# Kernel optimization log

Measured on AMD Instinct MI355X. Metric: run time of the kernel, lower is better.

## Reference

```python
import jax, jax.numpy as jnp
import numpy as np

N_NODES = 50000
N_EDGES = 500000
N_GRAPHS = 256
D_IN, D_H1, D_H2, D_H3, D_OUT = 768, 256, 128, 64, 2


def _glorot(key, shape):
    fan_in, fan_out = shape[1], shape[0]
    lim = float(np.sqrt(6.0 / (fan_in + fan_out)))
    return jax.random.uniform(key, shape, jnp.float32, -lim, lim)


def setup_inputs() -> dict:
    key = jax.random.key(0)
    ks = jax.random.split(key, 12)
    x = jax.random.normal(ks[0], (N_NODES, D_IN), jnp.float32)
    edge_index = jax.random.randint(ks[1], (2, N_EDGES), 0, N_NODES, jnp.int64)
    batch = jnp.sort(jax.random.randint(ks[2], (N_NODES,), 0, N_GRAPHS, jnp.int64))
    return {
        "x": x,
        "edge_index": edge_index,
        "batch": batch,
        # SAGEConv1: out = lin_l(mean_aggr) + lin_r(x); bias only on lin_l (PyG default)
        "W1_l": _glorot(ks[3], (D_H1, D_IN)),
        "b1_l": jnp.zeros((D_H1,), jnp.float32),
        "W1_r": _glorot(ks[4], (D_H1, D_IN)),
        # SAGEConv2
        "W2_l": _glorot(ks[5], (D_H2, D_H1)),
        "b2_l": jnp.zeros((D_H2,), jnp.float32),
        "W2_r": _glorot(ks[6], (D_H2, D_H1)),
        # MLP head
        "W3": _glorot(ks[7], (D_H3, D_H2)),
        "b3": jnp.zeros((D_H3,), jnp.float32),
        "W4": _glorot(ks[8], (D_OUT, D_H3)),
        "b4": jnp.zeros((D_OUT,), jnp.float32),
    }


def _sage_conv(x, src, dst, deg_inv, W_l, b_l, W_r):
    # mean aggregation of neighbor features: scatter-add then divide by in-degree
    aggr = jax.ops.segment_sum(x[src], dst, num_segments=N_NODES)  # [N, d]
    aggr = aggr * deg_inv[:, None]
    return aggr @ W_l.T + b_l + x @ W_r.T


def reference(x, edge_index, batch, W1_l, b1_l, W1_r, W2_l, b2_l, W2_r, W3, b3, W4, b4):
    src, dst = edge_index[0], edge_index[1]
    deg = jax.ops.segment_sum(jnp.ones((N_EDGES,), x.dtype), dst, num_segments=N_NODES)
    deg_inv = jnp.where(deg > 0, 1.0 / jnp.maximum(deg, 1.0), 0.0)

    h = jax.nn.relu(_sage_conv(x, src, dst, deg_inv, W1_l, b1_l, W1_r))
    h = jax.nn.relu(_sage_conv(h, src, dst, deg_inv, W2_l, b2_l, W2_r))

    # global_mean_pool over graph ids
    pooled = jax.ops.segment_sum(h, batch, num_segments=N_GRAPHS)  # [G, 128]
    cnt = jax.ops.segment_sum(jnp.ones((N_NODES,), h.dtype), batch, num_segments=N_GRAPHS)
    pooled = pooled / jnp.maximum(cnt, 1.0)[:, None]

    # dropout is identity in eval mode
    h = pooled @ W3.T + b3
    h = h @ W4.T + b4
    return jax.nn.softmax(h, axis=-1)
```

## Files before the change

### kernel.cpp

```cpp
#include <hip/hip_runtime.h>
#include <cstdint>
#include <cstddef>

#define N_NODES 50000
#define N_EDGES 500000
#define N_GRAPHS 256
#define D_IN 768
#define D_H1 256
#define D_H2 128

typedef __attribute__((ext_vector_type(8))) __bf16 bf16x8;
typedef __attribute__((ext_vector_type(4))) float f32x4;

__device__ __forceinline__ float bf2f(uint32_t u) {
    union { uint32_t i; float f; } v; v.i = u << 16; return v.f;
}
__device__ __forceinline__ uint32_t f2bf(float f) {
    union { float f; uint32_t i; } v; v.f = f;
    uint32_t u = v.i;
    return (u + 0x7FFFu + ((u >> 16) & 1u)) >> 16;
}

__device__ __forceinline__ void pack_chunk(const float* __restrict__ p,
                                           uint16_t* __restrict__ out, int c) {
    float4 u = *(const float4*)p, v = *(const float4*)(p + 4);
    uint4 o;
    o.x = f2bf(u.x) | (f2bf(u.y) << 16);
    o.y = f2bf(u.z) | (f2bf(u.w) << 16);
    o.z = f2bf(v.x) | (f2bf(v.y) << 16);
    o.w = f2bf(v.z) | (f2bf(v.w) << 16);
    *(uint4*)(out + (size_t)c * 8) = o;
}

#define PACKA_BLKS 18750
#define PACKW1_BLKS 192
#define PACKW2_BLKS 32
#define HIST_BLKS 1954
__global__ __launch_bounds__(256) void k_pack_hist(
    const float* __restrict__ x, uint16_t* __restrict__ xp,
    const float* __restrict__ W1l, const float* __restrict__ W1r, uint16_t* __restrict__ W1p,
    const float* __restrict__ W2l, const float* __restrict__ W2r, uint16_t* __restrict__ W2p,
    const int* __restrict__ e_dst, int* __restrict__ deg)
{
    int b = blockIdx.x;
    if (b < PACKA_BLKS) {
        int c = b * 256 + threadIdx.x;
        int l = c & 63, t = c >> 6;
        int kt = t % 24, mt = t / 24;
        int fr = l & 15, fq = l >> 4;
        pack_chunk(x + (size_t)(mt * 16 + fr) * 768 + kt * 32 + fq * 8, xp, c);
    } else if (b < PACKA_BLKS + PACKW1_BLKS) {
        int c = (b - PACKA_BLKS) * 256 + threadIdx.x;
        int l = c & 63, t = c >> 6;
        int kt = t % 24, mt = t / 24;
        int fr = l & 15, fq = l >> 4;
        int row = mt * 16 + fr;
        const float* src = (row < 256) ? (W1l + (size_t)row * 768)
                                       : (W1r + (size_t)(row - 256) * 768);
        pack_chunk(src + kt * 32 + fq * 8, W1p, c);
    } else if (b < PACKA_BLKS + PACKW1_BLKS + PACKW2_BLKS) {
        int c = (b - PACKA_BLKS - PACKW1_BLKS) * 256 + threadIdx.x;
        int l = c & 63, t = c >> 6;
        int kt = t % 8, mt = t / 8;
        int fr = l & 15, fq = l >> 4;
        int row = mt * 16 + fr;
        const float* src = (row < 128) ? (W2l + (size_t)row * 256)
                                       : (W2r + (size_t)(row - 128) * 256);
        pack_chunk(src + kt * 32 + fq * 8, W2p, c);
    } else {
        int e = (b - PACKA_BLKS - PACKW1_BLKS - PACKW2_BLKS) * 256 + threadIdx.x;
        if (e < N_EDGES) atomicAdd(&deg[e_dst[e]], 1);
    }
}

__global__ void k_scan1(const int* __restrict__ deg, int* __restrict__ row_ex,
                        int* __restrict__ bsum, int n) {
    __shared__ int buf[256];
    int t = threadIdx.x, i = blockIdx.x * 256 + t;
    int v = (i < n) ? deg[i] : 0;
    buf[t] = v; __syncthreads();
    for (int off = 1; off < 256; off <<= 1) {
        int u = (t >= off) ? buf[t - off] : 0;
        __syncthreads(); buf[t] += u; __syncthreads();
    }
    if (i < n) row_ex[i] = buf[t] - v;
    if (t == 255) bsum[blockIdx.x] = buf[255];
}
__global__ void k_scan23(const int* __restrict__ deg, const int* __restrict__ bsum,
                         int* __restrict__ row_start, float* __restrict__ deg_inv,
                         int n, int nb) {
    __shared__ int buf[256];
    int t = threadIdx.x;
    int v = (t < nb) ? bsum[t] : 0;
    buf[t] = v; __syncthreads();
    for (int off = 1; off < 256; off <<= 1) {
        int u = (t >= off) ? buf[t - off] : 0;
        __syncthreads(); buf[t] += u; __syncthreads();
    }
    int b = blockIdx.x;
    int boff = buf[b] - ((b < nb) ? bsum[b] : 0);
    int i = b * 256 + t;
    if (i < n) {
        row_start[i] += boff;
        int d = deg[i];
        deg_inv[i] = (d > 0) ? (1.0f / (float)d) : 0.0f;
    }
    if (b == 0 && t == 0) row_start[n] = N_EDGES;
}

#define G1_BLKS 784
__global__ __launch_bounds__(256, 2) void k_gemm1_fill(
    const uint16_t* __restrict__ Ap, const uint16_t* __restrict__ Bp,
    uint16_t* __restrict__ Cl, uint16_t* __restrict__ Cr,
    const int* __restrict__ e_src, const int* __restrict__ e_dst,
    const int* __restrict__ row_start, int* __restrict__ cursor,
    int* __restrict__ csr_src)
{
    if (blockIdx.x >= G1_BLKS) {
        int e = (blockIdx.x - G1_BLKS) * 256 + threadIdx.x;
        if (e < N_EDGES) {
            int d = e_dst[e];
            int pos = row_start[d] + atomicAdd(&cursor[d], 1);
            csr_src[pos] = e_src[e];
        }
        return;
    }
    const int i = blockIdx.x;
    const int pr = (i >> 4) * 8 + (i & 7);
    const int half = (i >> 3) & 1;
    if (pr >= 391) return;
    const int KT = 24, M = N_NODES;
    const int tid = threadIdx.x;
    const int wave = tid >> 6, lane = tid & 63;
    const int fr = lane & 15, fq = lane >> 4;
    const int bm = pr * 128;
    const int wm = (wave >> 1) * 64, wn = (wave & 1) * 128;
    const int mtiles = (M + 15) >> 4;

    const bf16x8* ap[4];
    const bf16x8* bp[8];
    #pragma unroll
    for (int mi = 0; mi < 4; ++mi) {
        int mt = ((bm + wm) >> 4) + mi;
        if (mt > mtiles - 1) mt = mtiles - 1;
        ap[mi] = (const bf16x8*)Ap + (size_t)mt * KT * 64 + lane;
    }
    #pragma unroll
    for (int ni = 0; ni < 8; ++ni) {
        int nt = ((half * 256 + wn) >> 4) + ni;
        bp[ni] = (const bf16x8*)Bp + (size_t)nt * KT * 64 + lane;
    }

    f32x4 acc[4][8] = {};
    bf16x8 a0[4], b0[8], a1[4], b1[8];

    auto lA = [&](int kt, bf16x8* d) {
        #pragma unroll
        for (int mi = 0; mi < 4; ++mi) d[mi] = ap[mi][kt * 64];
    };
    auto lB = [&](int kt, bf16x8* d) {
        #pragma unroll
        for (int ni = 0; ni < 8; ++ni) d[ni] = bp[ni][kt * 64];
    };
    auto step = [&](bf16x8* a, bf16x8* b) {
        #pragma unroll
        for (int mi = 0; mi < 4; ++mi)
            #pragma unroll
            for (int ni = 0; ni < 8; ++ni)
                acc[mi][ni] = __builtin_amdgcn_mfma_f32_16x16x32_bf16(
                    a[mi], b[ni], acc[mi][ni], 0, 0, 0);
    };

    lA(0, a0); lB(0, b0);
    for (int ks = 0; ks < KT; ks += 2) {
        lA(ks + 1, a1); lB(ks + 1, b1);
        step(a0, b0);
        if (ks + 2 < KT) { lA(ks + 2, a0); lB(ks + 2, b0); }
        step(a1, b1);
    }

    uint16_t* __restrict__ C = half ? Cr : Cl;
    #pragma unroll
    for (int mi = 0; mi < 4; ++mi) {
        #pragma unroll
        for (int r = 0; r < 4; ++r) {
            int row = bm + wm + mi * 16 + fq * 4 + r;
            if (row >= M) continue;
            #pragma unroll
            for (int ni = 0; ni < 8; ++ni) {
                int col = wn + ni * 16 + fr;
                C[(size_t)row * 256 + col] = (uint16_t)f2bf(acc[mi][ni][r]);
            }
        }
    }
}

__global__ __launch_bounds__(256, 2) void k_mgemm(
    const uint16_t* __restrict__ Ap, const uint16_t* __restrict__ Bp,
    uint16_t* __restrict__ C, int M, int N, int KT)
{
    const int tid = threadIdx.x;
    const int wave = tid >> 6, lane = tid & 63;
    const int fr = lane & 15, fq = lane >> 4;
    const int bn = blockIdx.x * 256, bm = blockIdx.y * 128;
    const int wm = (wave >> 1) * 64, wn = (wave & 1) * 128;
    const int mtiles = (M + 15) >> 4;

    const bf16x8* ap[4];
    const bf16x8* bp[8];
    #pragma unroll
    for (int mi = 0; mi < 4; ++mi) {
        int mt = ((bm + wm) >> 4) + mi;
        if (mt > mtiles - 1) mt = mtiles - 1;
        ap[mi] = (const bf16x8*)Ap + (size_t)mt * KT * 64 + lane;
    }
    #pragma unroll
    for (int ni = 0; ni < 8; ++ni) {
        int nt = ((bn + wn) >> 4) + ni;
        bp[ni] = (const bf16x8*)Bp + (size_t)nt * KT * 64 + lane;
    }

    f32x4 acc[4][8] = {};
    bf16x8 a0[4], b0[8], a1[4], b1[8];

    auto lA = [&](int kt, bf16x8* d) {
        #pragma unroll
        for (int mi = 0; mi < 4; ++mi) d[mi] = ap[mi][kt * 64];
    };
    auto lB = [&](int kt, bf16x8* d) {
        #pragma unroll
        for (int ni = 0; ni < 8; ++ni) d[ni] = bp[ni][kt * 64];
    };
    auto step = [&](bf16x8* a, bf16x8* b) {
        #pragma unroll
        for (int mi = 0; mi < 4; ++mi)
            #pragma unroll
            for (int ni = 0; ni < 8; ++ni)
                acc[mi][ni] = __builtin_amdgcn_mfma_f32_16x16x32_bf16(
                    a[mi], b[ni], acc[mi][ni], 0, 0, 0);
    };

    lA(0, a0); lB(0, b0);
    for (int ks = 0; ks < KT; ks += 2) {
        lA(ks + 1, a1); lB(ks + 1, b1);
        step(a0, b0);
        if (ks + 2 < KT) { lA(ks + 2, a0); lB(ks + 2, b0); }
        step(a1, b1);
    }

    #pragma unroll
    for (int mi = 0; mi < 4; ++mi) {
        #pragma unroll
        for (int r = 0; r < 4; ++r) {
            int row = bm + wm + mi * 16 + fq * 4 + r;
            if (row >= M) continue;
            #pragma unroll
            for (int ni = 0; ni < 8; ++ni) {
                int col = bn + wn + ni * 16 + fr;
                C[(size_t)row * N + col] = (uint16_t)f2bf(acc[mi][ni][r]);
            }
        }
    }
}

__global__ __launch_bounds__(256) void k_agg1(
    const uint16_t* __restrict__ yl, const uint16_t* __restrict__ yr,
    const int* __restrict__ row_start, const int* __restrict__ csr,
    const float* __restrict__ deg_inv, const float* __restrict__ bias,
    uint16_t* __restrict__ h1p)
{
    int node = blockIdx.x * 8 + (threadIdx.x >> 5);
    if (node >= N_NODES) return;
    int c = threadIdx.x & 31;
    int s = row_start[node], e = row_start[node + 1];
    float a[8] = {};
    int p = s;
    for (; p + 1 < e; p += 2) {
        uint4 t0 = *(const uint4*)(yl + (size_t)csr[p] * 256 + c * 8);
        uint4 t1 = *(const uint4*)(yl + (size_t)csr[p + 1] * 256 + c * 8);
        a[0] += bf2f(t0.x & 0xFFFF) + bf2f(t1.x & 0xFFFF);
        a[1] += bf2f(t0.x >> 16)    + bf2f(t1.x >> 16);
        a[2] += bf2f(t0.y & 0xFFFF) + bf2f(t1.y & 0xFFFF);
        a[3] += bf2f(t0.y >> 16)    + bf2f(t1.y >> 16);
        a[4] += bf2f(t0.z & 0xFFFF) + bf2f(t1.z & 0xFFFF);
        a[5] += bf2f(t0.z >> 16)    + bf2f(t1.z >> 16);
        a[6] += bf2f(t0.w & 0xFFFF) + bf2f(t1.w & 0xFFFF);
        a[7] += bf2f(t0.w >> 16)    + bf2f(t1.w >> 16);
    }
    if (p < e) {
        uint4 t0 = *(const uint4*)(yl + (size_t)csr[p] * 256 + c * 8);
        a[0] += bf2f(t0.x & 0xFFFF); a[1] += bf2f(t0.x >> 16);
        a[2] += bf2f(t0.y & 0xFFFF); a[3] += bf2f(t0.y >> 16);
        a[4] += bf2f(t0.z & 0xFFFF); a[5] += bf2f(t0.z >> 16);
        a[6] += bf2f(t0.w & 0xFFFF); a[7] += bf2f(t0.w >> 16);
    }
    float w = deg_inv[node];
    uint4 tx = *(const uint4*)(yr + (size_t)node * 256 + c * 8);
    float4 b0 = *(const float4*)(bias + c * 8);
    float4 b1 = *(const float4*)(bias + c * 8 + 4);
    float v0 = fmaxf(a[0] * w + bf2f(tx.x & 0xFFFF) + b0.x, 0.f);
    float v1 = fmaxf(a[1] * w + bf2f(tx.x >> 16)    + b0.y, 0.f);
    float v2 = fmaxf(a[2] * w + bf2f(tx.y & 0xFFFF) + b0.z, 0.f);
    float v3 = fmaxf(a[3] * w + bf2f(tx.y >> 16)    + b0.w, 0.f);
    float v4 = fmaxf(a[4] * w + bf2f(tx.z & 0xFFFF) + b1.x, 0.f);
    float v5 = fmaxf(a[5] * w + bf2f(tx.z >> 16)    + b1.y, 0.f);
    float v6 = fmaxf(a[6] * w + bf2f(tx.w & 0xFFFF) + b1.z, 0.f);
    float v7 = fmaxf(a[7] * w + bf2f(tx.w >> 16)    + b1.w, 0.f);
    uint4 o;
    o.x = f2bf(v0) | (f2bf(v1) << 16);
    o.y = f2bf(v2) | (f2bf(v3) << 16);
    o.z = f2bf(v4) | (f2bf(v5) << 16);
    o.w = f2bf(v6) | (f2bf(v7) << 16);
    uint32_t addr = (((node >> 4) * 8 + (c >> 2)) * 64 + (c & 3) * 16 + (node & 15));
    *(uint4*)(h1p + (size_t)addr * 8) = o;
}

__global__ __launch_bounds__(256) void k_agg2(
    const uint16_t* __restrict__ y, const int* __restrict__ row_start,
    const int* __restrict__ csr, const float* __restrict__ deg_inv,
    const float* __restrict__ bias, float* __restrict__ out)
{
    int node = blockIdx.x * 4 + (threadIdx.x >> 6);
    if (node >= N_NODES) return;
    int lane = threadIdx.x & 63;
    int s = row_start[node], e = row_start[node + 1];
    float a0 = 0.f, a1 = 0.f;
    int p = s;
    for (; p + 1 < e; p += 2) {
        uint32_t t0 = *(const uint32_t*)(y + (size_t)csr[p] * 256 + lane * 2);
        uint32_t t1 = *(const uint32_t*)(y + (size_t)csr[p + 1] * 256 + lane * 2);
        a0 += bf2f(t0 & 0xFFFF) + bf2f(t1 & 0xFFFF);
        a1 += bf2f(t0 >> 16)    + bf2f(t1 >> 16);
    }
    if (p < e) {
        uint32_t t0 = *(const uint32_t*)(y + (size_t)csr[p] * 256 + lane * 2);
        a0 += bf2f(t0 & 0xFFFF);
        a1 += bf2f(t0 >> 16);
    }
    float w = deg_inv[node];
    uint32_t tx = *(const uint32_t*)(y + (size_t)node * 256 + 128 + lane * 2);
    float2 b = *(const float2*)(bias + lane * 2);
    float2 o;
    o.x = fmaxf(a0 * w + bf2f(tx & 0xFFFF) + b.x, 0.f);
    o.y = fmaxf(a1 * w + bf2f(tx >> 16)    + b.y, 0.f);
    *(float2*)(out + (size_t)node * 128 + lane * 2) = o;
}

__global__ void k_poolhead(const float* __restrict__ h2, const int* __restrict__ batch,
                           const float* __restrict__ W3, const float* __restrict__ b3,
                           const float* __restrict__ W4, const float* __restrict__ b4,
                           float* __restrict__ out)
{
    int g = blockIdx.x;
    __shared__ int s_lo, s_hi;
    __shared__ float p[128];
    __shared__ float hid[64];
    __shared__ float logit[2];
    int t = threadIdx.x;
    if (t == 0) {
        int lo = 0, hi = N_NODES;
        while (lo < hi) { int m = (lo + hi) >> 1; if (batch[m] < g) lo = m + 1; else hi = m; }
        s_lo = lo;
        int lo2 = lo, hi2 = N_NODES;
        while (lo2 < hi2) { int m = (lo2 + hi2) >> 1; if (batch[m] < g + 1) lo2 = m + 1; else hi2 = m; }
        s_hi = lo2;
    }
    __syncthreads();
    float sum = 0.f;
    for (int i = s_lo; i < s_hi; ++i) sum += h2[(size_t)i * D_H2 + t];
    int cnt = s_hi - s_lo;
    p[t] = sum / (float)(cnt > 0 ? cnt : 1);
    __syncthreads();
    if (t < 64) {
        float s = b3[t];
        #pragma unroll 4
        for (int k = 0; k < 128; ++k) s = fmaf(p[k], W3[t * 128 + k], s);
        hid[t] = s;
    }
    __syncthreads();
    if (t < 2) {
        float l = b4[t];
        for (int k = 0; k < 64; ++k) l = fmaf(hid[k], W4[t * 64 + k], l);
        logit[t] = l;
    }
    __syncthreads();
    if (t == 0) {
        float m = fmaxf(logit[0], logit[1]);
        float e0 = expf(logit[0] - m), e1 = expf(logit[1] - m);
        float inv = 1.0f / (e0 + e1);
        out[g * 2 + 0] = e0 * inv;
        out[g * 2 + 1] = e1 * inv;
    }
}

extern "C" void kernel_launch(void* const* d_in, const int* in_sizes, int n_in,
                              void* d_out, int out_size, void* d_ws, size_t ws_size,
                              hipStream_t stream)
{
    const float* x     = (const float*)d_in[0];
    const int*   ei    = (const int*)d_in[1];
    const int*   batch = (const int*)d_in[2];
    const float* W1l   = (const float*)d_in[3];
    const float* b1l   = (const float*)d_in[4];
    const float* W1r   = (const float*)d_in[5];
    const float* W2l   = (const float*)d_in[6];
    const float* b2l   = (const float*)d_in[7];
    const float* W2r   = (const float*)d_in[8];
    const float* W3    = (const float*)d_in[9];
    const float* b3    = (const float*)d_in[10];
    const float* W4    = (const float*)d_in[11];
    const float* b4    = (const float*)d_in[12];
    float* out = (float*)d_out;

    const int* e_src = ei;
    const int* e_dst = ei + N_EDGES;

    char* ws = (char*)d_ws;
    size_t off = 0;
    auto alloc = [&](size_t bytes) -> void* {
        void* p = ws + off;
        off = (off + bytes + 255) & ~(size_t)255;
        return p;
    };
    int*      deg       = (int*)alloc((size_t)2 * N_NODES * 4);
    int*      cursor    = deg + N_NODES;
    int*      row_start = (int*)alloc((size_t)(N_NODES + 1) * 4);
    int*      csr_src   = (int*)alloc((size_t)N_EDGES * 4);
    float*    deg_inv   = (float*)alloc((size_t)N_NODES * 4);
    int*      bsum      = (int*)alloc(256 * 4);
    uint16_t* W1p       = (uint16_t*)alloc((size_t)512 * 768 * 2);
    uint16_t* W2p       = (uint16_t*)alloc((size_t)256 * 256 * 2);
    uint16_t* xp        = (uint16_t*)alloc((size_t)N_NODES * D_IN * 2);
    uint16_t* y1        = (uint16_t*)alloc((size_t)N_NODES * 512 * 2);
    uint16_t* h1p       = (uint16_t*)alloc((size_t)N_NODES * 256 * 2);

    uint16_t* y1l = y1;
    uint16_t* y1r = y1 + (size_t)N_NODES * 256;
    uint16_t* y2 = xp;
    float*    h2 = (float*)(xp + (size_t)N_NODES * 256);

    hipMemsetAsync(deg, 0, (size_t)2 * N_NODES * 4, stream);

    k_pack_hist<<<PACKA_BLKS + PACKW1_BLKS + PACKW2_BLKS + HIST_BLKS, 256, 0, stream>>>(
        x, xp, W1l, W1r, W1p, W2l, W2r, W2p, e_dst, deg);

    int nscan = (N_NODES + 255) / 256;
    k_scan1<<<nscan, 256, 0, stream>>>(deg, row_start, bsum, N_NODES);
    k_scan23<<<nscan, 256, 0, stream>>>(deg, bsum, row_start, deg_inv, N_NODES, nscan);

    k_gemm1_fill<<<G1_BLKS + HIST_BLKS, 256, 0, stream>>>(
        xp, W1p, y1l, y1r, e_src, e_dst, row_start, cursor, csr_src);
    k_agg1<<<(N_NODES + 7) / 8, 256, 0, stream>>>(y1l, y1r, row_start, csr_src, deg_inv, b1l, h1p);

    dim3 g2(1, (N_NODES + 127) / 128);
    k_mgemm<<<g2, 256, 0, stream>>>(h1p, W2p, y2, N_NODES, 256, 8);
    k_agg2<<<(N_NODES + 3) / 4, 256, 0, stream>>>(y2, row_start, csr_src, deg_inv, b2l, h2);

    k_poolhead<<<N_GRAPHS, 128, 0, stream>>>(h2, batch, W3, b3, W4, b4, out);
}
```

Measured before the change: 486.8 us.

## Fuse two-pass scan into one kernel with cross-block spin wait; unroll gathers by four

The two scan kernels become a single kernel. Each block publishes its block sum to a global array, and every block spin-waits on those sums to compute its own offset, which removes one launch. The scan also seeds the cursor array with the row start, so the CSR fill does one atomic instead of an extra row_start load. The aggregation loops are unrolled from two to four neighbours to put more loads in flight. The spin wait assumes all 196 scan blocks are co-resident, which holds on this GPU but is not guaranteed in general.

```diff
diff --git a/kernel.cpp b/kernel.cpp
--- a/kernel.cpp
+++ b/kernel.cpp
@@ -35,7 +35,7 @@
 #define PACKA_BLKS 18750
 #define PACKW1_BLKS 192
 #define PACKW2_BLKS 32
-#define HIST_BLKS 1954
+#define HIST256 1954
 __global__ __launch_bounds__(256) void k_pack_hist(
     const float* __restrict__ x, uint16_t* __restrict__ xp,
     const float* __restrict__ W1l, const float* __restrict__ W1r, uint16_t* __restrict__ W1p,
@@ -73,54 +73,53 @@
     }
 }
 
-__global__ void k_scan1(const int* __restrict__ deg, int* __restrict__ row_ex,
-                        int* __restrict__ bsum, int n) {
+__global__ __launch_bounds__(256) void k_scan(
+    const int* __restrict__ deg, int* __restrict__ row_start, int* __restrict__ cursor,
+    float* __restrict__ deg_inv, int* __restrict__ bsum, int n, int nb)
+{
     __shared__ int buf[256];
-    int t = threadIdx.x, i = blockIdx.x * 256 + t;
+    __shared__ int bbuf[256];
+    int t = threadIdx.x, b = blockIdx.x, i = b * 256 + t;
     int v = (i < n) ? deg[i] : 0;
     buf[t] = v; __syncthreads();
     for (int off = 1; off < 256; off <<= 1) {
         int u = (t >= off) ? buf[t - off] : 0;
         __syncthreads(); buf[t] += u; __syncthreads();
     }
-    if (i < n) row_ex[i] = buf[t] - v;
-    if (t == 255) bsum[blockIdx.x] = buf[255];
-}
-__global__ void k_scan23(const int* __restrict__ deg, const int* __restrict__ bsum,
-                         int* __restrict__ row_start, float* __restrict__ deg_inv,
-                         int n, int nb) {
-    __shared__ int buf[256];
-    int t = threadIdx.x;
-    int v = (t < nb) ? bsum[t] : 0;
-    buf[t] = v; __syncthreads();
+    if (t == 255) atomicExch(&bsum[b], buf[255] + 1);
+    int w = 0;
+    if (t < nb) {
+        do { w = atomicAdd(&bsum[t], 0); } while (w == 0);
+        w -= 1;
+    }
+    bbuf[t] = w; __syncthreads();
     for (int off = 1; off < 256; off <<= 1) {
-        int u = (t >= off) ? buf[t - off] : 0;
-        __syncthreads(); buf[t] += u; __syncthreads();
-    }
-    int b = blockIdx.x;
-    int boff = buf[b] - ((b < nb) ? bsum[b] : 0);
-    int i = b * 256 + t;
+        int u = (t >= off) ? bbuf[t - off] : 0;
+        __syncthreads(); bbuf[t] += u; __syncthreads();
+    }
+    int base = (b > 0) ? bbuf[b - 1] : 0;
     if (i < n) {
-        row_start[i] += boff;
-        int d = deg[i];
-        deg_inv[i] = (d > 0) ? (1.0f / (float)d) : 0.0f;
+        int rs = base + buf[t] - v;
+        row_start[i] = rs;
+        cursor[i] = rs;
+        deg_inv[i] = (v > 0) ? (1.0f / (float)v) : 0.0f;
     }
     if (b == 0 && t == 0) row_start[n] = N_EDGES;
 }
 
 #define G1_BLKS 784
+#define FILL_BLKS 1954
 __global__ __launch_bounds__(256, 2) void k_gemm1_fill(
     const uint16_t* __restrict__ Ap, const uint16_t* __restrict__ Bp,
     uint16_t* __restrict__ Cl, uint16_t* __restrict__ Cr,
     const int* __restrict__ e_src, const int* __restrict__ e_dst,
-    const int* __restrict__ row_start, int* __restrict__ cursor,
-    int* __restrict__ csr_src)
+    int* __restrict__ cursor, int* __restrict__ csr_src)
 {
     if (blockIdx.x >= G1_BLKS) {
         int e = (blockIdx.x - G1_BLKS) * 256 + threadIdx.x;
         if (e < N_EDGES) {
             int d = e_dst[e];
-            int pos = row_start[d] + atomicAdd(&cursor[d], 1);
+            int pos = atomicAdd(&cursor[d], 1);
             csr_src[pos] = e_src[e];
         }
         return;
@@ -129,13 +128,13 @@
     const int pr = (i >> 4) * 8 + (i & 7);
     const int half = (i >> 3) & 1;
     if (pr >= 391) return;
-    const int KT = 24, M = N_NODES;
+    const int KT = 24;
     const int tid = threadIdx.x;
     const int wave = tid >> 6, lane = tid & 63;
     const int fr = lane & 15, fq = lane >> 4;
     const int bm = pr * 128;
     const int wm = (wave >> 1) * 64, wn = (wave & 1) * 128;
-    const int mtiles = (M + 15) >> 4;
+    const int mtiles = (N_NODES + 15) >> 4;
 
     const bf16x8* ap[4];
     const bf16x8* bp[8];
@@ -185,7 +184,7 @@
         #pragma unroll
         for (int r = 0; r < 4; ++r) {
             int row = bm + wm + mi * 16 + fq * 4 + r;
-            if (row >= M) continue;
+            if (row >= N_NODES) continue;
             #pragma unroll
             for (int ni = 0; ni < 8; ++ni) {
                 int col = wn + ni * 16 + fr;
@@ -275,25 +274,21 @@
     int s = row_start[node], e = row_start[node + 1];
     float a[8] = {};
     int p = s;
-    for (; p + 1 < e; p += 2) {
-        uint4 t0 = *(const uint4*)(yl + (size_t)csr[p] * 256 + c * 8);
-        uint4 t1 = *(const uint4*)(yl + (size_t)csr[p + 1] * 256 + c * 8);
-        a[0] += bf2f(t0.x & 0xFFFF) + bf2f(t1.x & 0xFFFF);
-        a[1] += bf2f(t0.x >> 16)    + bf2f(t1.x >> 16);
-        a[2] += bf2f(t0.y & 0xFFFF) + bf2f(t1.y & 0xFFFF);
-        a[3] += bf2f(t0.y >> 16)    + bf2f(t1.y >> 16);
-        a[4] += bf2f(t0.z & 0xFFFF) + bf2f(t1.z & 0xFFFF);
-        a[5] += bf2f(t0.z >> 16)    + bf2f(t1.z >> 16);
-        a[6] += bf2f(t0.w & 0xFFFF) + bf2f(t1.w & 0xFFFF);
-        a[7] += bf2f(t0.w >> 16)    + bf2f(t1.w >> 16);
-    }
-    if (p < e) {
-        uint4 t0 = *(const uint4*)(yl + (size_t)csr[p] * 256 + c * 8);
+    auto accum = [&](uint4 t0) {
         a[0] += bf2f(t0.x & 0xFFFF); a[1] += bf2f(t0.x >> 16);
         a[2] += bf2f(t0.y & 0xFFFF); a[3] += bf2f(t0.y >> 16);
         a[4] += bf2f(t0.z & 0xFFFF); a[5] += bf2f(t0.z >> 16);
         a[6] += bf2f(t0.w & 0xFFFF); a[7] += bf2f(t0.w >> 16);
-    }
+    };
+    for (; p + 3 < e; p += 4) {
+        uint4 t0 = *(const uint4*)(yl + (size_t)csr[p]     * 256 + c * 8);
+        uint4 t1 = *(const uint4*)(yl + (size_t)csr[p + 1] * 256 + c * 8);
+        uint4 t2 = *(const uint4*)(yl + (size_t)csr[p + 2] * 256 + c * 8);
+        uint4 t3 = *(const uint4*)(yl + (size_t)csr[p + 3] * 256 + c * 8);
+        accum(t0); accum(t1); accum(t2); accum(t3);
+    }
+    for (; p < e; ++p)
+        accum(*(const uint4*)(yl + (size_t)csr[p] * 256 + c * 8));
     float w = deg_inv[node];
     uint4 tx = *(const uint4*)(yr + (size_t)node * 256 + c * 8);
     float4 b0 = *(const float4*)(bias + c * 8);
@@ -326,13 +321,15 @@
     int s = row_start[node], e = row_start[node + 1];
     float a0 = 0.f, a1 = 0.f;
     int p = s;
-    for (; p + 1 < e; p += 2) {
-        uint32_t t0 = *(const uint32_t*)(y + (size_t)csr[p] * 256 + lane * 2);
+    for (; p + 3 < e; p += 4) {
+        uint32_t t0 = *(const uint32_t*)(y + (size_t)csr[p]     * 256 + lane * 2);
         uint32_t t1 = *(const uint32_t*)(y + (size_t)csr[p + 1] * 256 + lane * 2);
-        a0 += bf2f(t0 & 0xFFFF) + bf2f(t1 & 0xFFFF);
-        a1 += bf2f(t0 >> 16)    + bf2f(t1 >> 16);
-    }
-    if (p < e) {
+        uint32_t t2 = *(const uint32_t*)(y + (size_t)csr[p + 2] * 256 + lane * 2);
+        uint32_t t3 = *(const uint32_t*)(y + (size_t)csr[p + 3] * 256 + lane * 2);
+        a0 += bf2f(t0 & 0xFFFF) + bf2f(t1 & 0xFFFF) + bf2f(t2 & 0xFFFF) + bf2f(t3 & 0xFFFF);
+        a1 += bf2f(t0 >> 16)    + bf2f(t1 >> 16)    + bf2f(t2 >> 16)    + bf2f(t3 >> 16);
+    }
+    for (; p < e; ++p) {
         uint32_t t0 = *(const uint32_t*)(y + (size_t)csr[p] * 256 + lane * 2);
         a0 += bf2f(t0 & 0xFFFF);
         a1 += bf2f(t0 >> 16);
@@ -422,12 +419,12 @@
         off = (off + bytes + 255) & ~(size_t)255;
         return p;
     };
-    int*      deg       = (int*)alloc((size_t)2 * N_NODES * 4);
-    int*      cursor    = deg + N_NODES;
+    int*      deg       = (int*)alloc((size_t)(N_NODES + 256) * 4);
+    int*      bsum      = deg + N_NODES;
     int*      row_start = (int*)alloc((size_t)(N_NODES + 1) * 4);
+    int*      cursor    = (int*)alloc((size_t)N_NODES * 4);
     int*      csr_src   = (int*)alloc((size_t)N_EDGES * 4);
     float*    deg_inv   = (float*)alloc((size_t)N_NODES * 4);
-    int*      bsum      = (int*)alloc(256 * 4);
     uint16_t* W1p       = (uint16_t*)alloc((size_t)512 * 768 * 2);
     uint16_t* W2p       = (uint16_t*)alloc((size_t)256 * 256 * 2);
     uint16_t* xp        = (uint16_t*)alloc((size_t)N_NODES * D_IN * 2);
@@ -439,17 +436,16 @@
     uint16_t* y2 = xp;
     float*    h2 = (float*)(xp + (size_t)N_NODES * 256);
 
-    hipMemsetAsync(deg, 0, (size_t)2 * N_NODES * 4, stream);
-
-    k_pack_hist<<<PACKA_BLKS + PACKW1_BLKS + PACKW2_BLKS + HIST_BLKS, 256, 0, stream>>>(
+    hipMemsetAsync(deg, 0, (size_t)(N_NODES + 256) * 4, stream);
+
+    k_pack_hist<<<PACKA_BLKS + PACKW1_BLKS + PACKW2_BLKS + HIST256, 256, 0, stream>>>(
         x, xp, W1l, W1r, W1p, W2l, W2r, W2p, e_dst, deg);
 
     int nscan = (N_NODES + 255) / 256;
-    k_scan1<<<nscan, 256, 0, stream>>>(deg, row_start, bsum, N_NODES);
-    k_scan23<<<nscan, 256, 0, stream>>>(deg, bsum, row_start, deg_inv, N_NODES, nscan);
-
-    k_gemm1_fill<<<G1_BLKS + HIST_BLKS, 256, 0, stream>>>(
-        xp, W1p, y1l, y1r, e_src, e_dst, row_start, cursor, csr_src);
+    k_scan<<<nscan, 256, 0, stream>>>(deg, row_start, cursor, deg_inv, bsum, N_NODES, nscan);
+
+    k_gemm1_fill<<<G1_BLKS + FILL_BLKS, 256, 0, stream>>>(
+        xp, W1p, y1l, y1r, e_src, e_dst, cursor, csr_src);
     k_agg1<<<(N_NODES + 7) / 8, 256, 0, stream>>>(y1l, y1r, row_start, csr_src, deg_inv, b1l, h1p);
 
     dim3 g2(1, (N_NODES + 127) / 128);
```

Result: no change. 481.9 us (-1.0%).
